# Kernel optimization log

Measured on AMD Instinct MI355X. Metric: run time of the kernel, lower is better.

## Reference

```python
import jax, jax.numpy as jnp
import numpy as np

STRIDE = 1
PADDING = 1

def setup_inputs() -> dict:
    key = jax.random.key(0)
    k1, k2 = jax.random.split(key)
    X = jax.random.normal(k1, (32, 1024, 1024), dtype=jnp.float32)
    weight = jnp.array([[-1.0, -1.0, -1.0], [-1.0, 8.0, -1.0], [-1.0, -1.0, -1.0]], dtype=jnp.float32)
    return {"X": X, "weight": weight}

def reference(X, weight):
    # single-channel 2D cross-correlation, stride=1, padding=1
    # X: [B, M, N] -> lhs [B, 1, M, N]; weight: [u, v] -> rhs [1, 1, u, v]
    lhs = X[:, None, :, :]
    rhs = weight[None, None, :, :]
    out = jax.lax.conv_general_dilated(
        lhs, rhs,
        window_strides=(STRIDE, STRIDE),
        padding=[(PADDING, PADDING), (PADDING, PADDING)],
        dimension_numbers=("NCHW", "OIHW", "NCHW"),
    )
    return out[:, 0, :, :]  # [B, out_h, out_w]
```

## Files before the change

kernel.cpp:

```cpp
#include <hip/hip_runtime.h>

#define IMG_W 1024
#define IMG_H 1024
#define BATCH 32
#define ROWS 8

typedef float vfloat4 __attribute__((ext_vector_type(4)));

__global__ __launch_bounds__(256) void conv3x3_kernel(
    const float* __restrict__ X,
    const float* __restrict__ wt,
    float* __restrict__ out)
{
    const int y0 = blockIdx.x * ROWS;
    const int b  = blockIdx.y;
    const int c0 = threadIdx.x * 4;

    const float* img = X + (size_t)b * IMG_H * IMG_W;

    const float w0 = wt[0], w1 = wt[1], w2 = wt[2];
    const float w3 = wt[3], w4 = wt[4], w5 = wt[5];
    const float w6 = wt[6], w7 = wt[7], w8 = wt[8];

    float R[ROWS + 2][6];

#pragma unroll
    for (int i = 0; i < ROWS + 2; ++i) {
        const int ry = y0 + i - 1;
        if (ry >= 0 && ry < IMG_H) {
            const float* p = img + (size_t)ry * IMG_W + c0;
            const vfloat4 v = *(const vfloat4*)p;
            R[i][1] = v.x; R[i][2] = v.y; R[i][3] = v.z; R[i][4] = v.w;
            R[i][0] = (c0 > 0)         ? p[-1] : 0.f;
            R[i][5] = (c0 + 4 < IMG_W) ? p[4]  : 0.f;
        } else {
            R[i][0] = R[i][1] = R[i][2] = R[i][3] = R[i][4] = R[i][5] = 0.f;
        }
    }

    float* obase = out + ((size_t)b * IMG_H + y0) * IMG_W + c0;

#pragma unroll
    for (int i = 0; i < ROWS; ++i) {
        vfloat4 r;
#pragma unroll
        for (int j = 0; j < 4; ++j) {
            r[j] = w0 * R[i][j]     + w1 * R[i][j + 1]     + w2 * R[i][j + 2]
                 + w3 * R[i + 1][j] + w4 * R[i + 1][j + 1] + w5 * R[i + 1][j + 2]
                 + w6 * R[i + 2][j] + w7 * R[i + 2][j + 1] + w8 * R[i + 2][j + 2];
        }
        __builtin_nontemporal_store(r, (vfloat4*)(obase + (size_t)i * IMG_W));
    }
}

extern "C" void kernel_launch(void* const* d_in, const int* in_sizes, int n_in,
                              void* d_out, int out_size, void* d_ws, size_t ws_size,
                              hipStream_t stream) {
    const float* X  = (const float*)d_in[0];
    const float* wt = (const float*)d_in[1];
    float* out = (float*)d_out;

    dim3 grid(IMG_H / ROWS, BATCH);
    dim3 block(256);
    conv3x3_kernel<<<grid, block, 0, stream>>>(X, wt, out);
}
```

Measured before the change: 229.6 us.

## Process taller row strips per block with a register-prefetched rolling window

```diff
diff --git a/kernel.cpp b/kernel.cpp
--- a/kernel.cpp
+++ b/kernel.cpp
@@ -3,16 +3,31 @@
 #define IMG_W 1024
 #define IMG_H 1024
 #define BATCH 32
-#define ROWS 8
+#define STRIP 32
+#define CHUNK 4
+#define NGROUP (STRIP / CHUNK)
 
 typedef float vfloat4 __attribute__((ext_vector_type(4)));
+
+__device__ __forceinline__ void load_row(const float* __restrict__ img, int ry,
+                                         int c0, float* dst) {
+    if (ry >= 0 && ry < IMG_H) {
+        const float* p = img + (size_t)ry * IMG_W + c0;
+        const vfloat4 v = *(const vfloat4*)p;
+        dst[1] = v.x; dst[2] = v.y; dst[3] = v.z; dst[4] = v.w;
+        dst[0] = (c0 > 0)         ? p[-1] : 0.f;
+        dst[5] = (c0 + 4 < IMG_W) ? p[4]  : 0.f;
+    } else {
+        dst[0] = dst[1] = dst[2] = dst[3] = dst[4] = dst[5] = 0.f;
+    }
+}
 
 __global__ __launch_bounds__(256) void conv3x3_kernel(
     const float* __restrict__ X,
     const float* __restrict__ wt,
     float* __restrict__ out)
 {
-    const int y0 = blockIdx.x * ROWS;
+    const int y0 = blockIdx.x * STRIP;
     const int b  = blockIdx.y;
     const int c0 = threadIdx.x * 4;
 
@@ -22,34 +37,45 @@
     const float w3 = wt[3], w4 = wt[4], w5 = wt[5];
     const float w6 = wt[6], w7 = wt[7], w8 = wt[8];
 
-    float R[ROWS + 2][6];
+    float W[CHUNK + 2][6];
+    float N[CHUNK][6];
 
 #pragma unroll
-    for (int i = 0; i < ROWS + 2; ++i) {
-        const int ry = y0 + i - 1;
-        if (ry >= 0 && ry < IMG_H) {
-            const float* p = img + (size_t)ry * IMG_W + c0;
-            const vfloat4 v = *(const vfloat4*)p;
-            R[i][1] = v.x; R[i][2] = v.y; R[i][3] = v.z; R[i][4] = v.w;
-            R[i][0] = (c0 > 0)         ? p[-1] : 0.f;
-            R[i][5] = (c0 + 4 < IMG_W) ? p[4]  : 0.f;
-        } else {
-            R[i][0] = R[i][1] = R[i][2] = R[i][3] = R[i][4] = R[i][5] = 0.f;
-        }
-    }
+    for (int i = 0; i < CHUNK + 2; ++i)
+        load_row(img, y0 - 1 + i, c0, W[i]);
 
     float* obase = out + ((size_t)b * IMG_H + y0) * IMG_W + c0;
 
+#pragma unroll 1
+    for (int g = 0; g < NGROUP; ++g) {
+        if (g + 1 < NGROUP) {
 #pragma unroll
-    for (int i = 0; i < ROWS; ++i) {
-        vfloat4 r;
+            for (int i = 0; i < CHUNK; ++i)
+                load_row(img, y0 + (g + 1) * CHUNK + 1 + i, c0, N[i]);
+        }
+
 #pragma unroll
-        for (int j = 0; j < 4; ++j) {
-            r[j] = w0 * R[i][j]     + w1 * R[i][j + 1]     + w2 * R[i][j + 2]
-                 + w3 * R[i + 1][j] + w4 * R[i + 1][j + 1] + w5 * R[i + 1][j + 2]
-                 + w6 * R[i + 2][j] + w7 * R[i + 2][j + 1] + w8 * R[i + 2][j + 2];
+        for (int i = 0; i < CHUNK; ++i) {
+            vfloat4 r;
+#pragma unroll
+            for (int j = 0; j < 4; ++j) {
+                r[j] = w0 * W[i][j]     + w1 * W[i][j + 1]     + w2 * W[i][j + 2]
+                     + w3 * W[i + 1][j] + w4 * W[i + 1][j + 1] + w5 * W[i + 1][j + 2]
+                     + w6 * W[i + 2][j] + w7 * W[i + 2][j + 1] + w8 * W[i + 2][j + 2];
+            }
+            __builtin_nontemporal_store(r, (vfloat4*)(obase + (size_t)(g * CHUNK + i) * IMG_W));
         }
-        __builtin_nontemporal_store(r, (vfloat4*)(obase + (size_t)i * IMG_W));
+
+#pragma unroll
+        for (int k = 0; k < 6; ++k) {
+            W[0][k] = W[CHUNK][k];
+            W[1][k] = W[CHUNK + 1][k];
+        }
+#pragma unroll
+        for (int i = 0; i < CHUNK; ++i)
+#pragma unroll
+            for (int k = 0; k < 6; ++k)
+                W[2 + i][k] = N[i][k];
     }
 }
 
@@ -60,7 +86,7 @@
     const float* wt = (const float*)d_in[1];
     float* out = (float*)d_out;
 
-    dim3 grid(IMG_H / ROWS, BATCH);
+    dim3 grid(IMG_H / STRIP, BATCH);
     dim3 block(256);
     conv3x3_kernel<<<grid, block, 0, stream>>>(X, wt, out);
 }
```

After: 239.9 us. 1.05x slower.
